# Kernel optimization log

Hardware: AMD Instinct MI355X
Metric: run time of the kernel (lower is better)

Reference implementation:

```python
import jax, jax.numpy as jnp
import numpy as np

S_LEN = 1024; HIDDEN = 2048; VOCAB = 32000; DFF = 6144
NK = 8; NV = 16; DK = 128; DV = 128; CONV_K = 4
CONV_DIM = 2 * NK * DK + NV * DV  # 4096
NQ = 16; NKV = 2; HD = 128; MAX_KV = 4096; SP = 512; CHUNK = 64


def silu(x):
    return x * jax.nn.sigmoid(x)


def rmsnorm(x, w, eps=1e-6):
    xf = x.astype(jnp.float32)
    return (xf * jax.lax.rsqrt(jnp.mean(xf * xf, -1, keepdims=True) + eps)) * w


def gated_rmsnorm(x, z, w, eps=1e-6):
    xf = x.astype(jnp.float32) * silu(z.astype(jnp.float32))
    return (xf * jax.lax.rsqrt(jnp.mean(xf * xf, -1, keepdims=True) + eps)) * w


def rotate_half(x):
    a, b = jnp.split(x, 2, -1)
    return jnp.concatenate([-b, a], -1)


def chunk_gated_delta_rule(q, k, v, g, beta, init_state, chunk=CHUNK):
    # q,k: [B,S,H,Dk]; v: [B,S,H,Dv]; g,beta: [B,S,H]; init_state: [B,H,Dk,Dv]
    q = q / jnp.sqrt(jnp.sum(q * q, -1, keepdims=True) + 1e-6)  # qk l2norm
    k = k / jnp.sqrt(jnp.sum(k * k, -1, keepdims=True) + 1e-6)
    tr = lambda x: x.transpose(0, 2, 1, 3).astype(jnp.float32)
    q, k, v = tr(q), tr(k), tr(v)
    g = g.transpose(0, 2, 1).astype(jnp.float32)
    beta = beta.transpose(0, 2, 1).astype(jnp.float32)
    B, H, S, Dk = q.shape
    Dv = v.shape[-1]
    N = S // chunk  # S is a multiple of chunk here (no padding needed)
    q = q * Dk ** -0.5
    rc = lambda x: x.reshape(B, H, N, chunk, x.shape[-1])
    q, k, v = rc(q), rc(k), rc(v)
    g = jnp.cumsum(g.reshape(B, H, N, chunk), -1)  # cumulative log-decay within chunk
    beta = beta.reshape(B, H, N, chunk)
    kb = k * beta[..., None]
    vb = v * beta[..., None]
    ii = jnp.arange(chunk)
    lower = ii[:, None] >= ii[None, :]
    strict = ii[:, None] > ii[None, :]
    decay = jnp.where(lower, jnp.exp(g[..., :, None] - g[..., None, :]), 0.0)
    # strictly-lower A; T = (I - A)^{-1} (exact triangular solve == converged Neumann series)
    A = -jnp.where(strict, jnp.einsum('bhnik,bhnjk->bhnij', kb, k) * decay, 0.0)
    eye = jnp.eye(chunk, dtype=jnp.float32)
    T = jax.scipy.linalg.solve_triangular(eye - A, jnp.broadcast_to(eye, A.shape), lower=True)
    w = jnp.einsum('bhnij,bhnjd->bhnid', T, vb)
    kc = jnp.einsum('bhnij,bhnjd->bhnid', T, kb * jnp.exp(g)[..., None])
    mv = lambda x: jnp.moveaxis(x, 2, 0)

    def step(state, xs):
        qi, ki, wi, kci, gi, di = xs
        attn = jnp.where(lower, jnp.einsum('bhik,bhjk->bhij', qi, ki) * di, 0.0)
        v_new = wi - jnp.einsum('bhik,bhkd->bhid', kci, state)
        out = jnp.einsum('bhik,bhkd->bhid', qi * jnp.exp(gi)[..., None], state) \
            + jnp.einsum('bhij,bhjd->bhid', attn, v_new)
        gl = gi[..., -1]
        kd = ki * jnp.exp(gl[..., None] - gi)[..., None]
        state = state * jnp.exp(gl)[..., None, None] + jnp.einsum('bhik,bhid->bhkd', kd, v_new)
        return state, out

    final, outs = jax.lax.scan(step, init_state.astype(jnp.float32),
                               (mv(q), mv(k), mv(w), mv(kc), mv(g), mv(decay)))
    out = jnp.moveaxis(outs, 0, 2).reshape(B, H, S, Dv).transpose(0, 2, 1, 3)  # [B,S,H,Dv]
    return out, final


def mlp(x, gw, uw, dw):
    return (silu(x @ gw) * (x @ uw)) @ dw


def model_forward(input_ids, start_pos, rope_cos, rope_sin, attn_mask, conv_state, rec_state,
                  key_cache, value_cache, embed_w, dl_ln_w, dl_qkv_w, conv_w, conv_b, dl_z_w,
                  dl_b_w, dl_a_w, A_log, dt_bias, dn_norm_w, dl_out_w, dl_post_ln_w, dl_gate_w,
                  dl_up_w, dl_down_w, al_ln_w, q_w, q_norm_w, k_w, k_norm_w, v_w, o_w,
                  al_post_ln_w, al_gate_w, al_up_w, al_down_w, final_norm_w, lm_head_w):
    B, S = input_ids.shape
    hidden = embed_w[input_ids]
    # ---------------- DeltaNet (linear attention) layer ----------------
    res = hidden
    x = rmsnorm(hidden, dl_ln_w)
    mixed = (x @ dl_qkv_w).transpose(0, 2, 1)             # [B, CONV_DIM, S]
    padded = jnp.concatenate([conv_state, mixed], -1)      # [B, CONV_DIM, K+S]
    L = padded.shape[-1] - (CONV_K - 1)
    conv = conv_b[:, None] + sum(conv_w[:, kk][:, None] * padded[:, :, kk:kk + L]
                                 for kk in range(CONV_K))  # depthwise conv1d
    mixed = silu(conv[:, :, -S:]).transpose(0, 2, 1)
    new_conv = padded[:, :, -CONV_K:]
    kd = NK * DK
    qq = mixed[..., :kd].reshape(B, S, NK, DK)
    kk_ = mixed[..., kd:2 * kd].reshape(B, S, NK, DK)
    vv = mixed[..., 2 * kd:].reshape(B, S, NV, DV)
    z = (x @ dl_z_w).reshape(B, S, NV, DV)
    beta = jax.nn.sigmoid(x @ dl_b_w)
    a = (x @ dl_a_w).astype(jnp.float32)
    g = -jnp.exp(A_log.astype(jnp.float32)) * jax.nn.softplus(a + dt_bias)
    rep = NV // NK
    qq = jnp.repeat(qq, rep, axis=2)
    kk_ = jnp.repeat(kk_, rep, axis=2)
    core, new_rec = chunk_gated_delta_rule(qq, kk_, vv, g, beta, rec_state)
    core = gated_rmsnorm(core.reshape(-1, DV), z.reshape(-1, DV), dn_norm_w).reshape(B, S, NV * DV)
    hidden = res + core @ dl_out_w
    hidden = hidden + mlp(rmsnorm(hidden, dl_post_ln_w), dl_gate_w, dl_up_w, dl_down_w)
    # ---------------- Full attention layer (gated GQA, KV-cache scatter) ----------------
    res = hidden
    x = rmsnorm(hidden, al_ln_w)
    qg = (x @ q_w).reshape(B, S, NQ, 2 * HD)
    query, gate = jnp.split(qg, 2, -1)
    gate = gate.reshape(B, S, NQ * HD)
    query = rmsnorm(query, q_norm_w).transpose(0, 2, 1, 3)               # [B,NQ,S,HD]
    key_new = rmsnorm((x @ k_w).reshape(B, S, NKV, HD), k_norm_w).transpose(0, 2, 1, 3)
    value_new = (x @ v_w).reshape(B, S, NKV, HD).transpose(0, 2, 1, 3)
    c = rope_cos[:, None]
    sn = rope_sin[:, None]
    query = query * c + rotate_half(query) * sn
    key_new = key_new * c + rotate_half(key_new) * sn
    new_kc = jax.lax.dynamic_update_slice(key_cache, key_new, (0, 0, start_pos, 0))
    new_vc = jax.lax.dynamic_update_slice(value_cache, value_new, (0, 0, start_pos, 0))
    ng = NQ // NKV
    k_rep = jnp.repeat(new_kc, ng, axis=1)
    v_rep = jnp.repeat(new_vc, ng, axis=1)
    scores = jnp.einsum('bhsd,bhtd->bhst', query, k_rep) * HD ** -0.5 + attn_mask
    probs = jax.nn.softmax(scores.astype(jnp.float32), -1).astype(query.dtype)
    ao = jnp.einsum('bhst,bhtd->bhsd', probs, v_rep).transpose(0, 2, 1, 3).reshape(B, S, NQ * HD)
    ao = ao * jax.nn.sigmoid(gate)
    hidden = res + ao @ o_w
    hidden = hidden + mlp(rmsnorm(hidden, al_post_ln_w), al_gate_w, al_up_w, al_down_w)
    logits = rmsnorm(hidden, final_norm_w) @ lm_head_w
    return logits, new_conv, new_rec, new_kc, new_vc


def setup_inputs():
    key = jax.random.key(0)
    ks = iter(jax.random.split(key, 64))
    def rn(shape, s=0.02):
        return jax.random.normal(next(ks), shape, jnp.float32) * s
    input_ids = jax.random.randint(next(ks), (1, S_LEN), 0, VOCAB)
    inv = 1.0 / (10000.0 ** (jnp.arange(0, HD, 2, dtype=jnp.float32) / HD))
    pos = jnp.arange(SP, SP + S_LEN, dtype=jnp.float32)
    fr = pos[:, None] * inv[None, :]
    emb = jnp.concatenate([fr, fr], -1)
    rope_cos = jnp.cos(emb)[None]
    rope_sin = jnp.sin(emb)[None]
    qpos = SP + jnp.arange(S_LEN)
    kpos = jnp.arange(MAX_KV)
    attn_mask = jnp.where(kpos[None, :] <= qpos[:, None], 0.0, -1e9).astype(jnp.float32)[None, None]
    return dict(
        input_ids=input_ids, seq_len=S_LEN, start_pos=SP,
        rope_cos=rope_cos, rope_sin=rope_sin, attn_mask=attn_mask,
        conv_state=rn((1, CONV_DIM, CONV_K), 1.0), rec_state=rn((1, NV, DK, DV), 1.0),
        key_cache=rn((1, NKV, MAX_KV, HD), 1.0), value_cache=rn((1, NKV, MAX_KV, HD), 1.0),
        embed_w=rn((VOCAB, HIDDEN)), dl_ln_w=jnp.ones(HIDDEN),
        dl_qkv_w=rn((HIDDEN, CONV_DIM)), conv_w=rn((CONV_DIM, CONV_K), 0.3),
        conv_b=rn((CONV_DIM,)), dl_z_w=rn((HIDDEN, NV * DV)),
        dl_b_w=rn((HIDDEN, NV)), dl_a_w=rn((HIDDEN, NV)),
        A_log=jnp.log(jnp.linspace(1.0, 8.0, NV)), dt_bias=rn((NV,), 0.1),
        dn_norm_w=jnp.ones(DV), dl_out_w=rn((NV * DV, HIDDEN)),
        dl_post_ln_w=jnp.ones(HIDDEN), dl_gate_w=rn((HIDDEN, DFF)),
        dl_up_w=rn((HIDDEN, DFF)), dl_down_w=rn((DFF, HIDDEN)),
        al_ln_w=jnp.ones(HIDDEN), q_w=rn((HIDDEN, NQ * HD * 2)), q_norm_w=jnp.ones(HD),
        k_w=rn((HIDDEN, NKV * HD)), k_norm_w=jnp.ones(HD), v_w=rn((HIDDEN, NKV * HD)),
        o_w=rn((NQ * HD, HIDDEN)), al_post_ln_w=jnp.ones(HIDDEN),
        al_gate_w=rn((HIDDEN, DFF)), al_up_w=rn((HIDDEN, DFF)), al_down_w=rn((DFF, HIDDEN)),
        final_norm_w=jnp.ones(HIDDEN), lm_head_w=rn((HIDDEN, VOCAB)))


def reference(input_ids, seq_len, start_pos, rope_cos, rope_sin, attn_mask, conv_state,
              rec_state, key_cache, value_cache, embed_w, dl_ln_w, dl_qkv_w, conv_w, conv_b,
              dl_z_w, dl_b_w, dl_a_w, A_log, dt_bias, dn_norm_w, dl_out_w, dl_post_ln_w,
              dl_gate_w, dl_up_w, dl_down_w, al_ln_w, q_w, q_norm_w, k_w, k_norm_w, v_w, o_w,
              al_post_ln_w, al_gate_w, al_up_w, al_down_w, final_norm_w, lm_head_w):
    del seq_len  # unused in original forward body (padding bookkeeping only)
    return model_forward(input_ids, start_pos, rope_cos, rope_sin, attn_mask, conv_state,
                         rec_state, key_cache, value_cache, embed_w, dl_ln_w, dl_qkv_w, conv_w,
                         conv_b, dl_z_w, dl_b_w, dl_a_w, A_log, dt_bias, dn_norm_w, dl_out_w,
                         dl_post_ln_w, dl_gate_w, dl_up_w, dl_down_w, al_ln_w, q_w, q_norm_w,
                         k_w, k_norm_w, v_w, o_w, al_post_ln_w, al_gate_w, al_up_w, al_down_w,
                         final_norm_w, lm_head_w)
```

## Files before the change

### kernel.cpp

```cpp
#include <hip/hip_runtime.h>
#include <math.h>

#define S_LEN 1024
#define HIDN  2048
#define NVH   16
#define CDIM  4096
#define MAXKV 4096
#define SP    512

typedef __attribute__((ext_vector_type(4))) float f32x4v;
typedef _Float16 f16x8 __attribute__((ext_vector_type(8)));
typedef unsigned short ushort_t;

__device__ __forceinline__ unsigned int pack2h(float a, float b) {
  auto h = __builtin_amdgcn_cvt_pkrtz(a, b);
  return __builtin_bit_cast(unsigned int, h);
}
__device__ __forceinline__ ushort_t h16(float x) {
  auto v = __builtin_amdgcn_cvt_pkrtz(x, x);
  return (ushort_t)__builtin_bit_cast(unsigned int, v);
}

template<bool ACC>
__global__ __launch_bounds__(256) void gemm_f16(const float* __restrict__ A,
    const float* __restrict__ B, float* __restrict__ C, int M, int N, int K) {
  __shared__ unsigned int Al[4][128][4];
  __shared__ unsigned int Bl[4][128][4];
  const int tid = threadIdx.x;
  const int gm = M >> 7;
  const int nwg = gridDim.x;
  const int q = nwg >> 3, r = nwg & 7;
  const int xcd = blockIdx.x & 7, ii = blockIdx.x >> 3;
  const int lin = (xcd < r) ? (xcd * (q + 1) + ii)
                            : (r * (q + 1) + (xcd - r) * q + ii);
  const int m0 = (lin % gm) * 128;
  const int n0 = (lin / gm) * 128;
  const int wave = tid >> 6, lane = tid & 63;
  const int wm = (wave >> 1) * 64, wn = (wave & 1) * 64;
  const int lr = lane & 15, lg = lane >> 4;
  const int am = tid >> 1, akb = (tid & 1) * 2;
  const int bn = tid & 127, bkb = (tid >> 7) * 2;
  const float* Ap = A + (size_t)(m0 + am) * K + akb * 8;
  const float* Bp = B + (size_t)(bkb * 8) * N + n0 + bn;
  float ar[16];
  float br[16];
  f32x4v acc[4][4];
  #pragma unroll
  for (int i = 0; i < 4; ++i)
    #pragma unroll
    for (int j = 0; j < 4; ++j)
      #pragma unroll
      for (int r2 = 0; r2 < 4; ++r2) acc[i][j][r2] = 0.f;
  const int NT = K >> 5;
  #pragma unroll
  for (int q2 = 0; q2 < 4; ++q2) *(float4*)&ar[q2 * 4] = *(const float4*)(Ap + q2 * 4);
  #pragma unroll
  for (int j = 0; j < 16; ++j) br[j] = Bp[(size_t)j * N];
  for (int t = 0; t < NT; ++t) {
    __syncthreads();
    *(uint4*)&Al[akb][am][0] = make_uint4(
        pack2h(ar[0], ar[1]), pack2h(ar[2], ar[3]),
        pack2h(ar[4], ar[5]), pack2h(ar[6], ar[7]));
    *(uint4*)&Al[akb + 1][am][0] = make_uint4(
        pack2h(ar[8], ar[9]), pack2h(ar[10], ar[11]),
        pack2h(ar[12], ar[13]), pack2h(ar[14], ar[15]));
    *(uint4*)&Bl[bkb][bn][0] = make_uint4(
        pack2h(br[0], br[1]), pack2h(br[2], br[3]),
        pack2h(br[4], br[5]), pack2h(br[6], br[7]));
    *(uint4*)&Bl[bkb + 1][bn][0] = make_uint4(
        pack2h(br[8], br[9]), pack2h(br[10], br[11]),
        pack2h(br[12], br[13]), pack2h(br[14], br[15]));
    if (t + 1 < NT) {
      Ap += 32; Bp += (size_t)32 * N;
      #pragma unroll
      for (int q2 = 0; q2 < 4; ++q2) *(float4*)&ar[q2 * 4] = *(const float4*)(Ap + q2 * 4);
      #pragma unroll
      for (int j = 0; j < 16; ++j) br[j] = Bp[(size_t)j * N];
    }
    __syncthreads();
    f16x8 af[4], bfr[4];
    #pragma unroll
    for (int mi = 0; mi < 4; ++mi)
      af[mi] = *(const f16x8*)&Al[lg][wm + mi * 16 + lr][0];
    #pragma unroll
    for (int ni = 0; ni < 4; ++ni)
      bfr[ni] = *(const f16x8*)&Bl[lg][wn + ni * 16 + lr][0];
    #pragma unroll
    for (int mi = 0; mi < 4; ++mi)
      #pragma unroll
      for (int ni = 0; ni < 4; ++ni)
        acc[mi][ni] = __builtin_amdgcn_mfma_f32_16x16x32_f16(
            af[mi], bfr[ni], acc[mi][ni], 0, 0, 0);
  }
  #pragma unroll
  for (int mi = 0; mi < 4; ++mi) {
    #pragma unroll
    for (int ni = 0; ni < 4; ++ni) {
      const int rr = m0 + wm + mi * 16 + lg * 4;
      const int cc = n0 + wn + ni * 16 + lr;
      #pragma unroll
      for (int r2 = 0; r2 < 4; ++r2) {
        float* cp = C + (size_t)(rr + r2) * N + cc;
        if (ACC) *cp += acc[mi][ni][r2];
        else     *cp = acc[mi][ni][r2];
      }
    }
  }
}

__global__ __launch_bounds__(256) void embed_k(const int* __restrict__ ids,
    const float* __restrict__ emb, float* __restrict__ hid) {
  int t = blockIdx.x * 256 + threadIdx.x;
  int s = t >> 9;
  int c4 = (t & 511) * 4;
  *(float4*)(hid + (size_t)s * HIDN + c4) =
      *(const float4*)(emb + (size_t)ids[s] * HIDN + c4);
}

__global__ __launch_bounds__(256) void rmsnorm_k(const float* __restrict__ in,
    const float* __restrict__ w, float* __restrict__ out) {
  const int row = blockIdx.x;
  const float* ip = in + (size_t)row * HIDN;
  float ss = 0.f;
  for (int c = threadIdx.x * 4; c < HIDN; c += 1024) {
    float4 v = *(const float4*)(ip + c);
    ss += v.x * v.x + v.y * v.y + v.z * v.z + v.w * v.w;
  }
  #pragma unroll
  for (int o = 32; o > 0; o >>= 1) ss += __shfl_down(ss, o, 64);
  __shared__ float sred[4];
  if ((threadIdx.x & 63) == 0) sred[threadIdx.x >> 6] = ss;
  __syncthreads();
  float tot = sred[0] + sred[1] + sred[2] + sred[3];
  float sc = 1.f / sqrtf(tot * (1.f / HIDN) + 1e-6f);
  for (int c = threadIdx.x * 4; c < HIDN; c += 1024) {
    float4 v = *(const float4*)(ip + c);
    float4 o = make_float4(v.x * sc * w[c], v.y * sc * w[c + 1],
                           v.z * sc * w[c + 2], v.w * sc * w[c + 3]);
    *(float4*)(out + (size_t)row * HIDN + c) = o;
  }
}

__global__ __launch_bounds__(256) void newconv_k(const float* __restrict__ mixed,
                                                 float* __restrict__ nc) {
  int t = blockIdx.x * 256 + threadIdx.x;
  int c = t >> 2, kk = t & 3;
  nc[t] = mixed[(size_t)(1020 + kk) * CDIM + c];
}

__global__ __launch_bounds__(256) void conv_k(const float* __restrict__ mixed,
    const float* __restrict__ cstate, const float* __restrict__ cw,
    const float* __restrict__ cb, float* __restrict__ convo) {
  int idx = blockIdx.x * 256 + threadIdx.x;
  int c = idx & (CDIM - 1);
  int s = idx >> 12;
  float acc = cb[c];
  #pragma unroll
  for (int kk = 0; kk < 4; ++kk) {
    int j = s + 1 + kk;
    float pv = (j < 4) ? cstate[c * 4 + j] : mixed[(size_t)(j - 4) * CDIM + c];
    acc = fmaf(cw[c * 4 + kk], pv, acc);
  }
  convo[(size_t)s * CDIM + c] = acc / (1.f + expf(-acc));
}

__global__ __launch_bounds__(128) void qknorm_k(const float* __restrict__ convo,
    float* __restrict__ qn, float* __restrict__ kn) {
  const int b = blockIdx.x;
  const int h8 = b & 7, s = b >> 3;
  const int d = threadIdx.x;
  float qv = convo[(size_t)s * CDIM + h8 * 128 + d];
  float kv = convo[(size_t)s * CDIM + 1024 + h8 * 128 + d];
  __shared__ float sred[4];
  float pq = qv * qv, pk = kv * kv;
  #pragma unroll
  for (int o = 32; o > 0; o >>= 1) { pq += __shfl_down(pq, o, 64); pk += __shfl_down(pk, o, 64); }
  if ((d & 63) == 0) { sred[d >> 6] = pq; sred[2 + (d >> 6)] = pk; }
  __syncthreads();
  float sq = sred[0] + sred[1], sk = sred[2] + sred[3];
  qn[((size_t)h8 * S_LEN + s) * 128 + d] = qv * (1.f / sqrtf(sq + 1e-6f)) * 0.08838834764831845f;
  kn[((size_t)h8 * S_LEN + s) * 128 + d] = kv * (1.f / sqrtf(sk + 1e-6f));
}

__global__ __launch_bounds__(256) void betag_k(const float* __restrict__ x,
    const float* __restrict__ bw, const float* __restrict__ aw,
    const float* __restrict__ A_log, const float* __restrict__ dt_bias,
    float* __restrict__ beta, float* __restrict__ g) {
  __shared__ float sx[2048];
  __shared__ float rb[16][17], ra[16][17];
  const int s = blockIdx.x;
  for (int c = threadIdx.x; c < HIDN; c += 256) sx[c] = x[(size_t)s * HIDN + c];
  __syncthreads();
  const int h = threadIdx.x & 15, part = threadIdx.x >> 4;
  float accb = 0.f, acca = 0.f;
  for (int j = 0; j < 128; ++j) {
    int k = part * 128 + j;
    float xv = sx[k];
    accb = fmaf(xv, bw[(size_t)k * 16 + h], accb);
    acca = fmaf(xv, aw[(size_t)k * 16 + h], acca);
  }
  rb[part][h] = accb; ra[part][h] = acca;
  __syncthreads();
  if (threadIdx.x < 16) {
    const int hh = threadIdx.x;
    float sb = 0.f, sa = 0.f;
    for (int p = 0; p < 16; ++p) { sb += rb[p][hh]; sa += ra[p][hh]; }
    beta[(size_t)s * 16 + hh] = 1.f / (1.f + expf(-sb));
    float aa = sa + dt_bias[hh];
    float sp = (aa > 20.f) ? aa : log1pf(expf(aa));
    g[(size_t)s * 16 + hh] = -expf(A_log[hh]) * sp;
  }
}

__global__ __launch_bounds__(256) void delta_phase1(
    const float* __restrict__ qn, const float* __restrict__ kn,
    const float* __restrict__ convo, const float* __restrict__ beta,
    const float* __restrict__ g,
    float* __restrict__ Wb, ushort_t* __restrict__ KC16,
    ushort_t* __restrict__ Q16, ushort_t* __restrict__ K16,
    ushort_t* __restrict__ ATT16, float* __restrict__ GCb) {
  __shared__ float sK[64][129];
  __shared__ float sV[64][129];
  __shared__ float sQ[64][129];
  __shared__ float sT[64][64];
  __shared__ float sgc[64], sbeta[64], seg[64], sEgl[64];
  const int blk = blockIdx.x;
  const int n = blk & 15, h = blk >> 4;
  const int hq = h >> 1;
  const int r0 = n * 64;
  const int tid = threadIdx.x;
  const size_t hn = (size_t)h * 16 + n;
  for (int t = tid; t < 2048; t += 256) {
    int i = t >> 5, c4 = (t & 31) * 4;
    float4 kv = *(const float4*)(kn + ((size_t)hq * S_LEN + r0 + i) * 128 + c4);
    float4 qv = *(const float4*)(qn + ((size_t)hq * S_LEN + r0 + i) * 128 + c4);
    float4 vv = *(const float4*)(convo + (size_t)(r0 + i) * CDIM + 2048 + h * 128 + c4);
    sK[i][c4+0]=kv.x; sK[i][c4+1]=kv.y; sK[i][c4+2]=kv.z; sK[i][c4+3]=kv.w;
    sQ[i][c4+0]=qv.x; sQ[i][c4+1]=qv.y; sQ[i][c4+2]=qv.z; sQ[i][c4+3]=qv.w;
    sV[i][c4+0]=vv.x; sV[i][c4+1]=vv.y; sV[i][c4+2]=vv.z; sV[i][c4+3]=vv.w;
  }
  if (tid < 64) sbeta[tid] = beta[(size_t)(r0 + tid) * NVH + h];
  __syncthreads();
  if (tid == 0) {
    float acc = 0.f;
    for (int i = 0; i < 64; ++i) { acc += g[(size_t)(r0 + i) * NVH + h]; sgc[i] = acc; }
  }
  __syncthreads();
  if (tid < 64) {
    seg[tid] = expf(sgc[tid]);
    sEgl[tid] = expf(sgc[63] - sgc[tid]);
  }
  {
    const int ty = tid >> 4, tx = tid & 15;
    float a[4][4] = {};
    #pragma unroll 4
    for (int k = 0; k < 128; ++k) {
      float kr[4], kc_[4];
      #pragma unroll
      for (int di = 0; di < 4; ++di) kr[di] = sK[ty * 4 + di][k];
      #pragma unroll
      for (int dj = 0; dj < 4; ++dj) kc_[dj] = sK[tx * 4 + dj][k];
      #pragma unroll
      for (int di = 0; di < 4; ++di)
        #pragma unroll
        for (int dj = 0; dj < 4; ++dj)
          a[di][dj] = fmaf(kr[di], kc_[dj], a[di][dj]);
    }
    #pragma unroll
    for (int di = 0; di < 4; ++di) {
      int i = ty * 4 + di;
      #pragma unroll
      for (int dj = 0; dj < 4; ++dj) {
        int j = tx * 4 + dj;
        float v;
        if (i > j) v = sbeta[i] * a[di][dj] * expf(sgc[i] - sgc[j]);
        else v = (i == j) ? 1.f : 0.f;
        sT[i][j] = v;
      }
    }
  }
  __syncthreads();
  for (int i = 1; i < 64; ++i) {
    float acc = 0.f;
    const int c = tid;
    const bool act = (c < 64 && c <= i);
    if (act) {
      acc = (c == i) ? 1.f : 0.f;
      for (int j = c; j < i; ++j) acc -= sT[i][j] * sT[j][c];
    }
    __syncthreads();
    if (act) sT[i][c] = acc;
    __syncthreads();
  }
  for (int t = tid; t < 1024; t += 256) {
    int i = t >> 4, dg = (t & 15) * 8;
    float aw[8] = {}, ak[8] = {};
    for (int j = 0; j <= i; ++j) {
      float tv = sT[i][j] * sbeta[j];
      float te = tv * seg[j];
      #pragma unroll
      for (int u = 0; u < 8; ++u) {
        aw[u] = fmaf(tv, sV[j][dg + u], aw[u]);
        ak[u] = fmaf(te, sK[j][dg + u], ak[u]);
      }
    }
    float* wp = Wb + (hn * 64 + i) * 128 + dg;
    *(float4*)wp = make_float4(aw[0], aw[1], aw[2], aw[3]);
    *(float4*)(wp + 4) = make_float4(aw[4], aw[5], aw[6], aw[7]);
    uint4 kc = make_uint4(pack2h(-ak[0], -ak[1]), pack2h(-ak[2], -ak[3]),
                          pack2h(-ak[4], -ak[5]), pack2h(-ak[6], -ak[7]));
    *(uint4*)(KC16 + hn * 8192 + (dg >> 3) * 512 + i * 8) = kc;
  }
  for (int t = tid; t < 1024; t += 256) {
    int i = t >> 4, dg = (t & 15) * 8;
    float e = seg[i];
    uint4 qv = make_uint4(
        pack2h(sQ[i][dg] * e, sQ[i][dg + 1] * e),
        pack2h(sQ[i][dg + 2] * e, sQ[i][dg + 3] * e),
        pack2h(sQ[i][dg + 4] * e, sQ[i][dg + 5] * e),
        pack2h(sQ[i][dg + 6] * e, sQ[i][dg + 7] * e));
    *(uint4*)(Q16 + hn * 8192 + (dg >> 3) * 512 + i * 8) = qv;
  }
  for (int t = tid; t < 1024; t += 256) {
    int kv = t & 127, ib = t >> 7;
    int i0 = ib * 8;
    uint4 kk2 = make_uint4(
        pack2h(sK[i0 + 0][kv] * sEgl[i0 + 0], sK[i0 + 1][kv] * sEgl[i0 + 1]),
        pack2h(sK[i0 + 2][kv] * sEgl[i0 + 2], sK[i0 + 3][kv] * sEgl[i0 + 3]),
        pack2h(sK[i0 + 4][kv] * sEgl[i0 + 4], sK[i0 + 5][kv] * sEgl[i0 + 5]),
        pack2h(sK[i0 + 6][kv] * sEgl[i0 + 6], sK[i0 + 7][kv] * sEgl[i0 + 7]));
    *(uint4*)(K16 + hn * 8192 + ib * 1024 + kv * 8) = kk2;
  }
  __syncthreads();
  {
    const int ty = tid >> 4, tx = tid & 15;
    float a[4][4] = {};
    #pragma unroll 4
    for (int k = 0; k < 128; ++k) {
      float qr[4], kc_[4];
      #pragma unroll
      for (int di = 0; di < 4; ++di) qr[di] = sQ[ty * 4 + di][k];
      #pragma unroll
      for (int dj = 0; dj < 4; ++dj) kc_[dj] = sK[tx * 4 + dj][k];
      #pragma unroll
      for (int di = 0; di < 4; ++di)
        #pragma unroll
        for (int dj = 0; dj < 4; ++dj)
          a[di][dj] = fmaf(qr[di], kc_[dj], a[di][dj]);
    }
    #pragma unroll
    for (int di = 0; di < 4; ++di) {
      int i = ty * 4 + di;
      #pragma unroll
      for (int dj = 0; dj < 4; ++dj) {
        int j = tx * 4 + dj;
        float v = 0.f;
        if (i >= j) v = a[di][dj] * expf(sgc[i] - sgc[j]);
        sT[i][j] = v;
      }
    }
  }
  __syncthreads();
  for (int t = tid; t < 512; t += 256) {
    int i = t >> 3, jb = t & 7;
    const float* ap = &sT[i][jb * 8];
    uint4 av = make_uint4(pack2h(ap[0], ap[1]), pack2h(ap[2], ap[3]),
                          pack2h(ap[4], ap[5]), pack2h(ap[6], ap[7]));
    *(uint4*)(ATT16 + hn * 4096 + jb * 512 + i * 8) = av;
  }
  if (tid < 64) GCb[hn * 64 + tid] = sgc[tid];
}

__global__ __launch_bounds__(256) void delta_phase2(
    const ushort_t* __restrict__ KC16, const ushort_t* __restrict__ Q16,
    const ushort_t* __restrict__ K16, const ushort_t* __restrict__ ATT16,
    const float* __restrict__ Wb, const float* __restrict__ GCb,
    const float* __restrict__ rec_state,
    float* __restrict__ core, float* __restrict__ new_rec) {
  __shared__ uint4 bufKC[1024];
  __shared__ uint4 bufQ[1024];
  __shared__ uint4 bufK[1024];
  __shared__ uint4 bufA[512];
  __shared__ uint4 bufS[512];
  __shared__ uint4 bufV[256];
  ushort_t* sKC = (ushort_t*)bufKC;
  ushort_t* sQ6 = (ushort_t*)bufQ;
  ushort_t* sK6 = (ushort_t*)bufK;
  ushort_t* sAT = (ushort_t*)bufA;
  ushort_t* sS  = (ushort_t*)bufS;
  ushort_t* sVn = (ushort_t*)bufV;
  const int h = blockIdx.x >> 2, ds = blockIdx.x & 3;
  const int d0 = ds * 32;
  const int tid = threadIdx.x;
  const int w = tid >> 6;
  const int lane = tid & 63, lr = lane & 15, lg = lane >> 4;
  const int rowS0 = w * 32;
  f32x4v aS[2][2];
  #pragma unroll
  for (int tm = 0; tm < 2; ++tm)
    #pragma unroll
    for (int tn = 0; tn < 2; ++tn)
      #pragma unroll
      for (int r = 0; r < 4; ++r) {
        int row = rowS0 + tm * 16 + lg * 4 + r;
        int col = tn * 16 + lr;
        aS[tm][tn][r] = rec_state[((size_t)h * 128 + row) * 128 + d0 + col];
      }
  for (int n = 0; n < 16; ++n) {
    const size_t hn = (size_t)h * 16 + n;
    const uint4* pKC = (const uint4*)(KC16 + hn * 8192);
    const uint4* pQ  = (const uint4*)(Q16  + hn * 8192);
    const uint4* pK  = (const uint4*)(K16  + hn * 8192);
    const uint4* pA  = (const uint4*)(ATT16 + hn * 4096);
    uint4 stKC[4], stQ[4], stK[4], stA[2];
    #pragma unroll
    for (int u = 0; u < 4; ++u) {
      stKC[u] = pKC[tid + u * 256];
      stQ[u]  = pQ[tid + u * 256];
      stK[u]  = pK[tid + u * 256];
    }
    #pragma unroll
    for (int u = 0; u < 2; ++u) stA[u] = pA[tid + u * 256];
    const float egl = expf(GCb[hn * 64 + 63]);
    float wseed[2][4];
    #pragma unroll
    for (int tn = 0; tn < 2; ++tn)
      #pragma unroll
      for (int r = 0; r < 4; ++r)
        wseed[tn][r] = Wb[(hn * 64 + (w * 16 + lg * 4 + r)) * 128 + d0 + tn * 16 + lr];
    #pragma unroll
    for (int tm = 0; tm < 2; ++tm)
      #pragma unroll
      for (int tn = 0; tn < 2; ++tn)
        #pragma unroll
        for (int r = 0; r < 4; ++r) {
          int row = rowS0 + tm * 16 + lg * 4 + r;
          int col = tn * 16 + lr;
          sS[(row >> 3) * 256 + col * 8 + (row & 7)] = h16(aS[tm][tn][r]);
        }
    #pragma unroll
    for (int u = 0; u < 4; ++u) {
      bufKC[tid + u * 256] = stKC[u];
      bufQ[tid + u * 256]  = stQ[u];
      bufK[tid + u * 256]  = stK[u];
    }
    #pragma unroll
    for (int u = 0; u < 2; ++u) bufA[tid + u * 256] = stA[u];
    __syncthreads();
    f32x4v aV[2];
    #pragma unroll
    for (int tn = 0; tn < 2; ++tn)
      #pragma unroll
      for (int r = 0; r < 4; ++r) aV[tn][r] = wseed[tn][r];
    #pragma unroll
    for (int c = 0; c < 4; ++c) {
      f16x8 a = *(const f16x8*)&sKC[((c * 4 + lg) * 64 + w * 16 + lr) * 8];
      #pragma unroll
      for (int tn = 0; tn < 2; ++tn) {
        f16x8 b = *(const f16x8*)&sS[((c * 4 + lg) * 32 + tn * 16 + lr) * 8];
        aV[tn] = __builtin_amdgcn_mfma_f32_16x16x32_f16(a, b, aV[tn], 0, 0, 0);
      }
    }
    #pragma unroll
    for (int tn = 0; tn < 2; ++tn)
      #pragma unroll
      for (int r = 0; r < 4; ++r) {
        int row = w * 16 + lg * 4 + r;
        int col = tn * 16 + lr;
        sVn[(row >> 3) * 256 + col * 8 + (row & 7)] = h16(aV[tn][r]);
      }
    __syncthreads();
    f32x4v aO[2];
    #pragma unroll
    for (int tn = 0; tn < 2; ++tn)
      #pragma unroll
      for (int r = 0; r < 4; ++r) aO[tn][r] = 0.f;
    #pragma unroll
    for (int c = 0; c < 4; ++c) {
      f16x8 a = *(const f16x8*)&sQ6[((c * 4 + lg) * 64 + w * 16 + lr) * 8];
      #pragma unroll
      for (int tn = 0; tn < 2; ++tn) {
        f16x8 b = *(const f16x8*)&sS[((c * 4 + lg) * 32 + tn * 16 + lr) * 8];
        aO[tn] = __builtin_amdgcn_mfma_f32_16x16x32_f16(a, b, aO[tn], 0, 0, 0);
      }
    }
    #pragma unroll
    for (int c = 0; c < 2; ++c) {
      f16x8 a = *(const f16x8*)&sAT[((c * 4 + lg) * 64 + w * 16 + lr) * 8];
      #pragma unroll
      for (int tn = 0; tn < 2; ++tn) {
        f16x8 b = *(const f16x8*)&sVn[((c * 4 + lg) * 32 + tn * 16 + lr) * 8];
        aO[tn] = __builtin_amdgcn_mfma_f32_16x16x32_f16(a, b, aO[tn], 0, 0, 0);
      }
    }
    #pragma unroll
    for (int tn = 0; tn < 2; ++tn)
      #pragma unroll
      for (int r = 0; r < 4; ++r) {
        int row = w * 16 + lg * 4 + r;
        core[(size_t)(n * 64 + row) * HIDN + h * 128 + d0 + tn * 16 + lr] = aO[tn][r];
      }
    #pragma unroll
    for (int tm = 0; tm < 2; ++tm)
      #pragma unroll
      for (int tn = 0; tn < 2; ++tn)
        #pragma unroll
        for (int r = 0; r < 4; ++r) aS[tm][tn][r] *= egl;
    #pragma unroll
    for (int tm = 0; tm < 2; ++tm) {
      #pragma unroll
      for (int c = 0; c < 2; ++c) {
        f16x8 a = *(const f16x8*)&sK6[((c * 4 + lg) * 128 + rowS0 + tm * 16 + lr) * 8];
        #pragma unroll
        for (int tn = 0; tn < 2; ++tn) {
          f16x8 b = *(const f16x8*)&sVn[((c * 4 + lg) * 32 + tn * 16 + lr) * 8];
          aS[tm][tn] = __builtin_amdgcn_mfma_f32_16x16x32_f16(a, b, aS[tm][tn], 0, 0, 0);
        }
      }
    }
    __syncthreads();
  }
  #pragma unroll
  for (int tm = 0; tm < 2; ++tm)
    #pragma unroll
    for (int tn = 0; tn < 2; ++tn)
      #pragma unroll
      for (int r = 0; r < 4; ++r) {
        int row = rowS0 + tm * 16 + lg * 4 + r;
        int col = tn * 16 + lr;
        new_rec[((size_t)h * 128 + row) * 128 + d0 + col] = aS[tm][tn][r];
      }
}

__global__ __launch_bounds__(128) void gatedrms_k(float* __restrict__ core,
    const float* __restrict__ z, const float* __restrict__ w) {
  const int b = blockIdx.x;
  const int h = b & 15, s = b >> 4;
  const int d = threadIdx.x;
  size_t idx = (size_t)s * HIDN + h * 128 + d;
  float cv = core[idx], zv = z[idx];
  float xf = cv * (zv / (1.f + expf(-zv)));
  __shared__ float sred[2];
  float ps = xf * xf;
  #pragma unroll
  for (int o = 32; o > 0; o >>= 1) ps += __shfl_down(ps, o, 64);
  if ((d & 63) == 0) sred[d >> 6] = ps;
  __syncthreads();
  float ss = sred[0] + sred[1];
  core[idx] = xf * (1.f / sqrtf(ss * (1.f / 128.f) + 1e-6f)) * w[d];
}

__global__ __launch_bounds__(256) void silumul_k(float* __restrict__ gbuf,
                                                 const float* __restrict__ ubuf) {
  int t = blockIdx.x * 256 + threadIdx.x;
  float4 gv = ((const float4*)gbuf)[t];
  float4 uv = ((const float4*)ubuf)[t];
  gv.x = gv.x / (1.f + expf(-gv.x)) * uv.x;
  gv.y = gv.y / (1.f + expf(-gv.y)) * uv.y;
  gv.z = gv.z / (1.f + expf(-gv.z)) * uv.z;
  gv.w = gv.w / (1.f + expf(-gv.w)) * uv.w;
  ((float4*)gbuf)[t] = gv;
}

__global__ __launch_bounds__(128) void qrope_k(const float* __restrict__ qg,
    const float* __restrict__ qnw, const float* __restrict__ cosb,
    const float* __restrict__ sinb, float* __restrict__ qhat,
    float* __restrict__ agate) {
  const int b = blockIdx.x;
  const int h = b & 15, s = b >> 4;
  const int d = threadIdx.x;
  float qv = qg[(size_t)s * 4096 + h * 256 + d];
  float gv = qg[(size_t)s * 4096 + h * 256 + 128 + d];
  __shared__ float sred[2];
  float ps = qv * qv;
  #pragma unroll
  for (int o = 32; o > 0; o >>= 1) ps += __shfl_down(ps, o, 64);
  if ((d & 63) == 0) sred[d >> 6] = ps;
  __syncthreads();
  float ss = sred[0] + sred[1];
  float qn_ = qv * (1.f / sqrtf(ss * (1.f / 128.f) + 1e-6f)) * qnw[d];
  __shared__ float tmp[128];
  tmp[d] = qn_;
  __syncthreads();
  float other = tmp[d ^ 64];
  float rh = (d < 64) ? -other : other;
  float c = cosb[(size_t)s * 128 + d];
  float sn = sinb[(size_t)s * 128 + d];
  qhat[((size_t)h * S_LEN + s) * 128 + d] = qn_ * c + rh * sn;
  agate[(size_t)s * HIDN + h * 128 + d] = gv;
}

__global__ __launch_bounds__(128) void kvrope_k(const float* __restrict__ kraw,
    const float* __restrict__ vraw, const float* __restrict__ knw,
    const float* __restrict__ cosb, const float* __restrict__ sinb,
    float* __restrict__ kcache, float* __restrict__ vcache) {
  const int b = blockIdx.x;
  const int h2 = b & 1, s = b >> 1;
  const int d = threadIdx.x;
  float kv = kraw[(size_t)s * 256 + h2 * 128 + d];
  __shared__ float sred[2];
  float ps = kv * kv;
  #pragma unroll
  for (int o = 32; o > 0; o >>= 1) ps += __shfl_down(ps, o, 64);
  if ((d & 63) == 0) sred[d >> 6] = ps;
  __syncthreads();
  float ss = sred[0] + sred[1];
  float kn_ = kv * (1.f / sqrtf(ss * (1.f / 128.f) + 1e-6f)) * knw[d];
  __shared__ float tmp[128];
  tmp[d] = kn_;
  __syncthreads();
  float other = tmp[d ^ 64];
  float rh = (d < 64) ? -other : other;
  size_t row = (size_t)h2 * MAXKV + SP + s;
  kcache[row * 128 + d] = kn_ * cosb[(size_t)s * 128 + d] + rh * sinb[(size_t)s * 128 + d];
  vcache[row * 128 + d] = vraw[(size_t)s * 256 + h2 * 128 + d];
}

__global__ __launch_bounds__(256) void attn_k(const float* __restrict__ qhat,
    const float* __restrict__ kcache, const float* __restrict__ vcache,
    const float* __restrict__ agate, float* __restrict__ ao) {
  __shared__ unsigned int Ql[16][64][4];
  __shared__ unsigned int Kl[16][64][4];
  __shared__ unsigned int Vl[8][128][4];
  __shared__ unsigned int Pl[8][64][4];
  const int h = blockIdx.x >> 4, qb = blockIdx.x & 15;
  const int hkv = h >> 3;
  const int tid = threadIdx.x;
  const int wave = tid >> 6, lane = tid & 63;
  const int lr = lane & 15, lg = lane >> 4;
  const float SCALE = 0.08838834764831845f;
  const float* Qb = qhat + ((size_t)h * S_LEN + qb * 64) * 128;
  #pragma unroll
  for (int it = 0; it < 4; ++it) {
    int tt = tid + it * 256;
    int row = tt >> 4, kb = tt & 15;
    float4 a = *(const float4*)(Qb + row * 128 + kb * 8);
    float4 b = *(const float4*)(Qb + row * 128 + kb * 8 + 4);
    *(uint4*)&Ql[kb][row][0] = make_uint4(
        pack2h(a.x * SCALE, a.y * SCALE), pack2h(a.z * SCALE, a.w * SCALE),
        pack2h(b.x * SCALE, b.y * SCALE), pack2h(b.z * SCALE, b.w * SCALE));
  }
  float m_run[4], l_run[4];
  #pragma unroll
  for (int r = 0; r < 4; ++r) { m_run[r] = -3.0e38f; l_run[r] = 0.f; }
  f32x4v accO[8];
  #pragma unroll
  for (int nd = 0; nd < 8; ++nd)
    #pragma unroll
    for (int r = 0; r < 4; ++r) accO[nd][r] = 0.f;
  const int ntiles = 9 + qb;
  for (int kt = 0; kt < ntiles; ++kt) {
    __syncthreads();
    const float* Kb = kcache + ((size_t)hkv * MAXKV + kt * 64) * 128;
    const float* Vb = vcache + ((size_t)hkv * MAXKV + kt * 64) * 128;
    #pragma unroll
    for (int it = 0; it < 4; ++it) {
      int tt = tid + it * 256;
      int row = tt >> 4, kb = tt & 15;
      float4 a = *(const float4*)(Kb + row * 128 + kb * 8);
      float4 b = *(const float4*)(Kb + row * 128 + kb * 8 + 4);
      *(uint4*)&Kl[kb][row][0] = make_uint4(
          pack2h(a.x, a.y), pack2h(a.z, a.w), pack2h(b.x, b.y), pack2h(b.z, b.w));
    }
    #pragma unroll
    for (int it = 0; it < 4; ++it) {
      int tt = tid + it * 256;
      int key = tt >> 4, dg = tt & 15;
      float4 a = *(const float4*)(Vb + key * 128 + dg * 8);
      float4 b = *(const float4*)(Vb + key * 128 + dg * 8 + 4);
      _Float16* vp = (_Float16*)Vl;
      int base = (key >> 3) * 1024 + (key & 7);
      vp[base + (dg * 8 + 0) * 8] = (_Float16)a.x;
      vp[base + (dg * 8 + 1) * 8] = (_Float16)a.y;
      vp[base + (dg * 8 + 2) * 8] = (_Float16)a.z;
      vp[base + (dg * 8 + 3) * 8] = (_Float16)a.w;
      vp[base + (dg * 8 + 4) * 8] = (_Float16)b.x;
      vp[base + (dg * 8 + 5) * 8] = (_Float16)b.y;
      vp[base + (dg * 8 + 6) * 8] = (_Float16)b.z;
      vp[base + (dg * 8 + 7) * 8] = (_Float16)b.w;
    }
    __syncthreads();
    f32x4v accS[4];
    #pragma unroll
    for (int ni = 0; ni < 4; ++ni)
      #pragma unroll
      for (int r = 0; r < 4; ++r) accS[ni][r] = 0.f;
    #pragma unroll
    for (int c = 0; c < 4; ++c) {
      f16x8 aq = *(const f16x8*)&Ql[c * 4 + lg][wave * 16 + lr][0];
      #pragma unroll
      for (int ni = 0; ni < 4; ++ni) {
        f16x8 bk = *(const f16x8*)&Kl[c * 4 + lg][ni * 16 + lr][0];
        accS[ni] = __builtin_amdgcn_mfma_f32_16x16x32_f16(aq, bk, accS[ni], 0, 0, 0);
      }
    }
    const bool boundary = (kt == ntiles - 1);
    float alpha[4];
    #pragma unroll
    for (int r = 0; r < 4; ++r) {
      const int qrow = wave * 16 + lg * 4 + r;
      float tm = -3.0e38f;
      #pragma unroll
      for (int ni = 0; ni < 4; ++ni) {
        if (boundary && (ni * 16 + lr) > qrow) accS[ni][r] = -3.0e38f;
        tm = fmaxf(tm, accS[ni][r]);
      }
      tm = fmaxf(tm, __shfl_xor(tm, 1, 64));
      tm = fmaxf(tm, __shfl_xor(tm, 2, 64));
      tm = fmaxf(tm, __shfl_xor(tm, 4, 64));
      tm = fmaxf(tm, __shfl_xor(tm, 8, 64));
      float mnew = fmaxf(m_run[r], tm);
      alpha[r] = expf(m_run[r] - mnew);
      m_run[r] = mnew;
      float ls = 0.f;
      #pragma unroll
      for (int ni = 0; ni < 4; ++ni) {
        float p = expf(accS[ni][r] - mnew);
        accS[ni][r] = p;
        ls += p;
      }
      ls += __shfl_xor(ls, 1, 64);
      ls += __shfl_xor(ls, 2, 64);
      ls += __shfl_xor(ls, 4, 64);
      ls += __shfl_xor(ls, 8, 64);
      l_run[r] = l_run[r] * alpha[r] + ls;
    }
    {
      _Float16* pp = (_Float16*)Pl;
      #pragma unroll
      for (int ni = 0; ni < 4; ++ni) {
        int key = ni * 16 + lr;
        int base = (key >> 3) * 512 + (key & 7);
        #pragma unroll
        for (int r = 0; r < 4; ++r) {
          int q = wave * 16 + lg * 4 + r;
          pp[base + q * 8] = (_Float16)accS[ni][r];
        }
      }
    }
    #pragma unroll
    for (int nd = 0; nd < 8; ++nd)
      #pragma unroll
      for (int r = 0; r < 4; ++r) accO[nd][r] *= alpha[r];
    #pragma unroll
    for (int c2 = 0; c2 < 2; ++c2) {
      f16x8 ap = *(const f16x8*)&Pl[c2 * 4 + lg][wave * 16 + lr][0];
      #pragma unroll
      for (int nd = 0; nd < 8; ++nd) {
        f16x8 bv = *(const f16x8*)&Vl[c2 * 4 + lg][nd * 16 + lr][0];
        accO[nd] = __builtin_amdgcn_mfma_f32_16x16x32_f16(ap, bv, accO[nd], 0, 0, 0);
      }
    }
  }
  #pragma unroll
  for (int r = 0; r < 4; ++r) {
    const int s = qb * 64 + wave * 16 + lg * 4 + r;
    const float inv = 1.f / l_run[r];
    #pragma unroll
    for (int nd = 0; nd < 8; ++nd) {
      int d = nd * 16 + lr;
      float gv = agate[(size_t)s * HIDN + h * 128 + d];
      ao[(size_t)s * HIDN + h * 128 + d] = accO[nd][r] * inv * (1.f / (1.f + expf(-gv)));
    }
  }
}

static inline void gemm(const float* A, const float* B, float* C,
                        int M, int N, int K, bool acc, hipStream_t st) {
  dim3 g((N / 128) * (M / 128));
  if (acc) hipLaunchKernelGGL((gemm_f16<true>),  g, dim3(256), 0, st, A, B, C, M, N, K);
  else     hipLaunchKernelGGL((gemm_f16<false>), g, dim3(256), 0, st, A, B, C, M, N, K);
}

extern "C" void kernel_launch(void* const* d_in, const int* in_sizes, int n_in,
                              void* d_out, int out_size, void* d_ws, size_t ws_size,
                              hipStream_t stream) {
  (void)in_sizes; (void)n_in; (void)out_size; (void)ws_size;
  const int*   ids         = (const int*)  d_in[0];
  const float* rope_cos    = (const float*)d_in[3];
  const float* rope_sin    = (const float*)d_in[4];
  const float* conv_state  = (const float*)d_in[6];
  const float* rec_state   = (const float*)d_in[7];
  const float* key_cache   = (const float*)d_in[8];
  const float* value_cache = (const float*)d_in[9];
  const float* embed_w     = (const float*)d_in[10];
  const float* dl_ln_w     = (const float*)d_in[11];
  const float* dl_qkv_w    = (const float*)d_in[12];
  const float* conv_w      = (const float*)d_in[13];
  const float* conv_b      = (const float*)d_in[14];
  const float* dl_z_w      = (const float*)d_in[15];
  const float* dl_b_w      = (const float*)d_in[16];
  const float* dl_a_w      = (const float*)d_in[17];
  const float* A_log       = (const float*)d_in[18];
  const float* dt_bias     = (const float*)d_in[19];
  const float* dn_norm_w   = (const float*)d_in[20];
  const float* dl_out_w    = (const float*)d_in[21];
  const float* dl_post_ln  = (const float*)d_in[22];
  const float* dl_gate_w   = (const float*)d_in[23];
  const float* dl_up_w     = (const float*)d_in[24];
  const float* dl_down_w   = (const float*)d_in[25];
  const float* al_ln_w     = (const float*)d_in[26];
  const float* q_w         = (const float*)d_in[27];
  const float* q_norm_w    = (const float*)d_in[28];
  const float* k_w         = (const float*)d_in[29];
  const float* k_norm_w    = (const float*)d_in[30];
  const float* v_w         = (const float*)d_in[31];
  const float* o_w         = (const float*)d_in[32];
  const float* al_post_ln  = (const float*)d_in[33];
  const float* al_gate_w   = (const float*)d_in[34];
  const float* al_up_w     = (const float*)d_in[35];
  const float* al_down_w   = (const float*)d_in[36];
  const float* final_norm  = (const float*)d_in[37];
  const float* lm_head_w   = (const float*)d_in[38];

  float* out = (float*)d_out;
  float* logits   = out;
  float* new_conv = out + 32768000;
  float* new_rec  = out + 32784384;
  float* new_kc   = out + 33046528;
  float* new_vc   = out + 34095104;

  float* A_mixed = logits;
  float* A_convo = logits + 4194304;
  float* A_z     = logits + 8388608;
  float* A_qn    = logits + 10485760;
  float* A_kn    = logits + 11534336;
  float* A_w     = logits + 12582912;
  float* A_kc    = logits + 14680064;
  float* A_att   = logits + 16777216;
  float* A_gc    = logits + 17825792;
  float* A_core  = logits + 17842176;
  float* A_big0  = logits + 19939328;
  float* A_big1  = logits + 26230784;
  float* A_qhat  = A_big1;
  float* A_gate  = A_big1 + 2097152;
  float* A_ao    = A_big1 + 4194304;
  float* A_kraw  = A_mixed;
  float* A_vraw  = A_mixed + 262144;

  ushort_t* KC16  = (ushort_t*)A_kc;
  ushort_t* K16   = (ushort_t*)A_kc + 2097152;
  ushort_t* Q16   = (ushort_t*)A_att;
  ushort_t* ATT16 = (ushort_t*)A_big0;

  float* ws     = (float*)d_ws;
  float* W_hid  = ws;
  float* W_x    = ws + 2097152;
  float* W_beta = ws + 4194304;
  float* W_g    = ws + 4210688;

  hipLaunchKernelGGL(embed_k, dim3(2048), dim3(256), 0, stream, ids, embed_w, W_hid);
  hipLaunchKernelGGL(rmsnorm_k, dim3(1024), dim3(256), 0, stream, W_hid, dl_ln_w, W_x);
  gemm(W_x, dl_qkv_w, A_mixed, 1024, 4096, 2048, false, stream);
  hipLaunchKernelGGL(newconv_k, dim3(64), dim3(256), 0, stream, A_mixed, new_conv);
  hipLaunchKernelGGL(conv_k, dim3(16384), dim3(256), 0, stream,
                     A_mixed, conv_state, conv_w, conv_b, A_convo);
  gemm(W_x, dl_z_w, A_z, 1024, 2048, 2048, false, stream);
  hipLaunchKernelGGL(betag_k, dim3(1024), dim3(256), 0, stream,
                     W_x, dl_b_w, dl_a_w, A_log, dt_bias, W_beta, W_g);
  hipLaunchKernelGGL(qknorm_k, dim3(8192), dim3(128), 0, stream, A_convo, A_qn, A_kn);
  hipLaunchKernelGGL(delta_phase1, dim3(256), dim3(256), 0, stream,
                     A_qn, A_kn, A_convo, W_beta, W_g,
                     A_w, KC16, Q16, K16, ATT16, A_gc);
  hipLaunchKernelGGL(delta_phase2, dim3(64), dim3(256), 0, stream,
                     KC16, Q16, K16, ATT16, A_w, A_gc, rec_state, A_core, new_rec);
  hipLaunchKernelGGL(gatedrms_k, dim3(16384), dim3(128), 0, stream, A_core, A_z, dn_norm_w);
  gemm(A_core, dl_out_w, W_hid, 1024, 2048, 2048, true, stream);
  hipLaunchKernelGGL(rmsnorm_k, dim3(1024), dim3(256), 0, stream, W_hid, dl_post_ln, W_x);
  gemm(W_x, dl_gate_w, A_big0, 1024, 6144, 2048, false, stream);
  gemm(W_x, dl_up_w,   A_big1, 1024, 6144, 2048, false, stream);
  hipLaunchKernelGGL(silumul_k, dim3(6144), dim3(256), 0, stream, A_big0, A_big1);
  gemm(A_big0, dl_down_w, W_hid, 1024, 2048, 6144, true, stream);
  hipLaunchKernelGGL(rmsnorm_k, dim3(1024), dim3(256), 0, stream, W_hid, al_ln_w, W_x);
  gemm(W_x, q_w, A_big0, 1024, 4096, 2048, false, stream);
  hipLaunchKernelGGL(qrope_k, dim3(16384), dim3(128), 0, stream,
                     A_big0, q_norm_w, rope_cos, rope_sin, A_qhat, A_gate);
  gemm(W_x, k_w, A_kraw, 1024, 256, 2048, false, stream);
  gemm(W_x, v_w, A_vraw, 1024, 256, 2048, false, stream);
  hipMemcpyAsync(new_kc, key_cache,   (size_t)2 * MAXKV * 128 * 4, hipMemcpyDeviceToDevice, stream);
  hipMemcpyAsync(new_vc, value_cache, (size_t)2 * MAXKV * 128 * 4, hipMemcpyDeviceToDevice, stream);
  hipLaunchKernelGGL(kvrope_k, dim3(2048), dim3(128), 0, stream,
                     A_kraw, A_vraw, k_norm_w, rope_cos, rope_sin, new_kc, new_vc);
  hipLaunchKernelGGL(attn_k, dim3(256), dim3(256), 0, stream,
                     A_qhat, new_kc, new_vc, A_gate, A_ao);
  gemm(A_ao, o_w, W_hid, 1024, 2048, 2048, true, stream);
  hipLaunchKernelGGL(rmsnorm_k, dim3(1024), dim3(256), 0, stream, W_hid, al_post_ln, W_x);
  gemm(W_x, al_gate_w, A_big0, 1024, 6144, 2048, false, stream);
  gemm(W_x, al_up_w,   A_big1, 1024, 6144, 2048, false, stream);
  hipLaunchKernelGGL(silumul_k, dim3(6144), dim3(256), 0, stream, A_big0, A_big1);
  gemm(A_big0, al_down_w, W_hid, 1024, 2048, 6144, true, stream);
  hipLaunchKernelGGL(rmsnorm_k, dim3(1024), dim3(256), 0, stream, W_hid, final_norm, W_x);
  gemm(W_x, lm_head_w, logits, 1024, 32000, 2048, false, stream);
}
```

Before: 1.719 ms.

## Pre-convert weights to tiled fp16 and stream B tiles directly into LDS

Before each GEMM, a new kernel converts that layer's fp32 weight matrix into a pre-tiled fp16 buffer held in a large device global. The GEMM then loads B tiles with global_load_lds 16-byte direct-to-LDS copies instead of strided per-column fp32 loads plus in-register packing. This targets the uncoalesced, repeated fp32 weight reads that every row-tile block performed. The cost is an extra full read of all fp32 weights and an fp16 write every call, about 343 MB of added device global state, and reliance on correct vmcnt waits before the barrier for the async LDS loads.

Result: slower. 2.032 ms (+18.2%).

```diff
diff --git a/kernel.cpp b/kernel.cpp
--- a/kernel.cpp
+++ b/kernel.cpp
@@ -12,6 +12,9 @@
 typedef _Float16 f16x8 __attribute__((ext_vector_type(8)));
 typedef unsigned short ushort_t;
 
+#define W16_TOTAL 171442176ULL
+__device__ ushort_t g_W16[W16_TOTAL];
+
 __device__ __forceinline__ unsigned int pack2h(float a, float b) {
   auto h = __builtin_amdgcn_cvt_pkrtz(a, b);
   return __builtin_bit_cast(unsigned int, h);
@@ -20,12 +23,40 @@
   auto v = __builtin_amdgcn_cvt_pkrtz(x, x);
   return (ushort_t)__builtin_bit_cast(unsigned int, v);
 }
+__device__ __forceinline__ void gload16(const void* g, void* l) {
+  __builtin_amdgcn_global_load_lds(
+      (const __attribute__((address_space(1))) void*)(g),
+      (__attribute__((address_space(3))) void*)(l), 16, 0, 0);
+}
+
+__global__ __launch_bounds__(256) void convw_k(const float* __restrict__ W,
+    size_t off, int K, int N, int total) {
+  int t = blockIdx.x * 256 + threadIdx.x;
+  if (t >= total) return;
+  int n_glob = t % N;
+  int kb_glob = t / N;
+  int kt = kb_glob >> 2, kb = kb_glob & 3;
+  int np = n_glob >> 7, n = n_glob & 127;
+  const float* src = W + (size_t)(kt * 32 + kb * 8) * N + n_glob;
+  float v0 = src[0];
+  float v1 = src[(size_t)N];
+  float v2 = src[(size_t)2 * N];
+  float v3 = src[(size_t)3 * N];
+  float v4 = src[(size_t)4 * N];
+  float v5 = src[(size_t)5 * N];
+  float v6 = src[(size_t)6 * N];
+  float v7 = src[(size_t)7 * N];
+  uint4 o = make_uint4(pack2h(v0, v1), pack2h(v2, v3),
+                       pack2h(v4, v5), pack2h(v6, v7));
+  *(uint4*)(g_W16 + off + ((size_t)np * (K >> 5) + kt) * 4096
+            + (size_t)((kb << 7) + n) * 8) = o;
+}
 
 template<bool ACC>
 __global__ __launch_bounds__(256) void gemm_f16(const float* __restrict__ A,
-    const float* __restrict__ B, float* __restrict__ C, int M, int N, int K) {
+    size_t bOff, float* __restrict__ C, int M, int N, int K) {
   __shared__ unsigned int Al[4][128][4];
-  __shared__ unsigned int Bl[4][128][4];
+  __shared__ unsigned int Bl[2048];
   const int tid = threadIdx.x;
   const int gm = M >> 7;
   const int nwg = gridDim.x;
@@ -39,11 +70,9 @@
   const int wm = (wave >> 1) * 64, wn = (wave & 1) * 64;
   const int lr = lane & 15, lg = lane >> 4;
   const int am = tid >> 1, akb = (tid & 1) * 2;
-  const int bn = tid & 127, bkb = (tid >> 7) * 2;
   const float* Ap = A + (size_t)(m0 + am) * K + akb * 8;
-  const float* Bp = B + (size_t)(bkb * 8) * N + n0 + bn;
+  const ushort_t* Bt = g_W16 + bOff + (size_t)(n0 >> 7) * (K >> 5) * 4096;
   float ar[16];
-  float br[16];
   f32x4v acc[4][4];
   #pragma unroll
   for (int i = 0; i < 4; ++i)
@@ -54,28 +83,26 @@
   const int NT = K >> 5;
   #pragma unroll
   for (int q2 = 0; q2 < 4; ++q2) *(float4*)&ar[q2 * 4] = *(const float4*)(Ap + q2 * 4);
-  #pragma unroll
-  for (int j = 0; j < 16; ++j) br[j] = Bp[(size_t)j * N];
   for (int t = 0; t < NT; ++t) {
     __syncthreads();
+    {
+      const ushort_t* bs = Bt + (size_t)t * 4096;
+      #pragma unroll
+      for (int i2 = 0; i2 < 2; ++i2) {
+        int c = wave * 2 + i2;
+        gload16(bs + c * 512 + lane * 8, &Bl[c * 256]);
+      }
+    }
     *(uint4*)&Al[akb][am][0] = make_uint4(
         pack2h(ar[0], ar[1]), pack2h(ar[2], ar[3]),
         pack2h(ar[4], ar[5]), pack2h(ar[6], ar[7]));
     *(uint4*)&Al[akb + 1][am][0] = make_uint4(
         pack2h(ar[8], ar[9]), pack2h(ar[10], ar[11]),
         pack2h(ar[12], ar[13]), pack2h(ar[14], ar[15]));
-    *(uint4*)&Bl[bkb][bn][0] = make_uint4(
-        pack2h(br[0], br[1]), pack2h(br[2], br[3]),
-        pack2h(br[4], br[5]), pack2h(br[6], br[7]));
-    *(uint4*)&Bl[bkb + 1][bn][0] = make_uint4(
-        pack2h(br[8], br[9]), pack2h(br[10], br[11]),
-        pack2h(br[12], br[13]), pack2h(br[14], br[15]));
     if (t + 1 < NT) {
-      Ap += 32; Bp += (size_t)32 * N;
+      Ap += 32;
       #pragma unroll
       for (int q2 = 0; q2 < 4; ++q2) *(float4*)&ar[q2 * 4] = *(const float4*)(Ap + q2 * 4);
-      #pragma unroll
-      for (int j = 0; j < 16; ++j) br[j] = Bp[(size_t)j * N];
     }
     __syncthreads();
     f16x8 af[4], bfr[4];
@@ -84,7 +111,7 @@
       af[mi] = *(const f16x8*)&Al[lg][wm + mi * 16 + lr][0];
     #pragma unroll
     for (int ni = 0; ni < 4; ++ni)
-      bfr[ni] = *(const f16x8*)&Bl[lg][wn + ni * 16 + lr][0];
+      bfr[ni] = *(const f16x8*)&Bl[(lg * 128 + wn + ni * 16 + lr) * 4];
     #pragma unroll
     for (int mi = 0; mi < 4; ++mi)
       #pragma unroll
@@ -765,11 +792,31 @@
   }
 }
 
-static inline void gemm(const float* A, const float* B, float* C,
+#define OFF_QKV 0ULL
+#define OFF_Z   8388608ULL
+#define OFF_OUT 12582912ULL
+#define OFF_G1  16777216ULL
+#define OFF_U1  29360128ULL
+#define OFF_D1  41943040ULL
+#define OFF_Q   54525952ULL
+#define OFF_K   62914560ULL
+#define OFF_V   63438848ULL
+#define OFF_O   63963136ULL
+#define OFF_G2  68157440ULL
+#define OFF_U2  80740352ULL
+#define OFF_D2  93323264ULL
+#define OFF_LM  105906176ULL
+
+static inline void convw(const float* W, size_t off, int K, int N, hipStream_t st) {
+  int total = (K >> 3) * N;
+  hipLaunchKernelGGL(convw_k, dim3((total + 255) / 256), dim3(256), 0, st,
+                     W, off, K, N, total);
+}
+static inline void gemm(const float* A, size_t bOff, float* C,
                         int M, int N, int K, bool acc, hipStream_t st) {
   dim3 g((N / 128) * (M / 128));
-  if (acc) hipLaunchKernelGGL((gemm_f16<true>),  g, dim3(256), 0, st, A, B, C, M, N, K);
-  else     hipLaunchKernelGGL((gemm_f16<false>), g, dim3(256), 0, st, A, B, C, M, N, K);
+  if (acc) hipLaunchKernelGGL((gemm_f16<true>),  g, dim3(256), 0, st, A, bOff, C, M, N, K);
+  else     hipLaunchKernelGGL((gemm_f16<false>), g, dim3(256), 0, st, A, bOff, C, M, N, K);
 }
 
 extern "C" void kernel_launch(void* const* d_in, const int* in_sizes, int n_in,
@@ -851,11 +898,13 @@
 
   hipLaunchKernelGGL(embed_k, dim3(2048), dim3(256), 0, stream, ids, embed_w, W_hid);
   hipLaunchKernelGGL(rmsnorm_k, dim3(1024), dim3(256), 0, stream, W_hid, dl_ln_w, W_x);
-  gemm(W_x, dl_qkv_w, A_mixed, 1024, 4096, 2048, false, stream);
+  convw(dl_qkv_w, OFF_QKV, 2048, 4096, stream);
+  gemm(W_x, OFF_QKV, A_mixed, 1024, 4096, 2048, false, stream);
   hipLaunchKernelGGL(newconv_k, dim3(64), dim3(256), 0, stream, A_mixed, new_conv);
   hipLaunchKernelGGL(conv_k, dim3(16384), dim3(256), 0, stream,
                      A_mixed, conv_state, conv_w, conv_b, A_convo);
-  gemm(W_x, dl_z_w, A_z, 1024, 2048, 2048, false, stream);
+  convw(dl_z_w, OFF_Z, 2048, 2048, stream);
+  gemm(W_x, OFF_Z, A_z, 1024, 2048, 2048, false, stream);
   hipLaunchKernelGGL(betag_k, dim3(1024), dim3(256), 0, stream,
                      W_x, dl_b_w, dl_a_w, A_log, dt_bias, W_beta, W_g);
   hipLaunchKernelGGL(qknorm_k, dim3(8192), dim3(128), 0, stream, A_convo, A_qn, A_kn);
@@ -865,30 +914,42 @@
   hipLaunchKernelGGL(delta_phase2, dim3(64), dim3(256), 0, stream,
                      KC16, Q16, K16, ATT16, A_w, A_gc, rec_state, A_core, new_rec);
   hipLaunchKernelGGL(gatedrms_k, dim3(16384), dim3(128), 0, stream, A_core, A_z, dn_norm_w);
-  gemm(A_core, dl_out_w, W_hid, 1024, 2048, 2048, true, stream);
+  convw(dl_out_w, OFF_OUT, 2048, 2048, stream);
+  gemm(A_core, OFF_OUT, W_hid, 1024, 2048, 2048, true, stream);
   hipLaunchKernelGGL(rmsnorm_k, dim3(1024), dim3(256), 0, stream, W_hid, dl_post_ln, W_x);
-  gemm(W_x, dl_gate_w, A_big0, 1024, 6144, 2048, false, stream);
-  gemm(W_x, dl_up_w,   A_big1, 1024, 6144, 2048, false, stream);
+  convw(dl_gate_w, OFF_G1, 2048, 6144, stream);
+  gemm(W_x, OFF_G1, A_big0, 1024, 6144, 2048, false, stream);
+  convw(dl_up_w, OFF_U1, 2048, 6144, stream);
+  gemm(W_x, OFF_U1, A_big1, 1024, 6144, 2048, false, stream);
   hipLaunchKernelGGL(silumul_k, dim3(6144), dim3(256), 0, stream, A_big0, A_big1);
-  gemm(A_big0, dl_down_w, W_hid, 1024, 2048, 6144, true, stream);
+  convw(dl_down_w, OFF_D1, 6144, 2048, stream);
+  gemm(A_big0, OFF_D1, W_hid, 1024, 2048, 6144, true, stream);
   hipLaunchKernelGGL(rmsnorm_k, dim3(1024), dim3(256), 0, stream, W_hid, al_ln_w, W_x);
-  gemm(W_x, q_w, A_big0, 1024, 4096, 2048, false, stream);
+  convw(q_w, OFF_Q, 2048, 4096, stream);
+  gemm(W_x, OFF_Q, A_big0, 1024, 4096, 2048, false, stream);
   hipLaunchKernelGGL(qrope_k, dim3(16384), dim3(128), 0, stream,
                      A_big0, q_norm_w, rope_cos, rope_sin, A_qhat, A_gate);
-  gemm(W_x, k_w, A_kraw, 1024, 256, 2048, false, stream);
-  gemm(W_x, v_w, A_vraw, 1024, 256, 2048, false, stream);
+  convw(k_w, OFF_K, 2048, 256, stream);
+  gemm(W_x, OFF_K, A_kraw, 1024, 256, 2048, false, stream);
+  convw(v_w, OFF_V, 2048, 256, stream);
+  gemm(W_x, OFF_V, A_vraw, 1024, 256, 2048, false, stream);
   hipMemcpyAsync(new_kc, key_cache,   (size_t)2 * MAXKV * 128 * 4, hipMemcpyDeviceToDevice, stream);
   hipMemcpyAsync(new_vc, value_cache, (size_t)2 * MAXKV * 128 * 4, hipMemcpyDeviceToDevice, stream);
   hipLaunchKernelGGL(kvrope_k, dim3(2048), dim3(128), 0, stream,
                      A_kraw, A_vraw, k_norm_w, rope_cos, rope_sin, new_kc, new_vc);
   hipLaunchKernelGGL(attn_k, dim3(256), dim3(256), 0, stream,
                      A_qhat, new_kc, new_vc, A_gate, A_ao);
-  gemm(A_ao, o_w, W_hid, 1024, 2048, 2048, true, stream);
+  convw(o_w, OFF_O, 2048, 2048, stream);
+  gemm(A_ao, OFF_O, W_hid, 1024, 2048, 2048, true, stream);
   hipLaunchKernelGGL(rmsnorm_k, dim3(1024), dim3(256), 0, stream, W_hid, al_post_ln, W_x);
-  gemm(W_x, al_gate_w, A_big0, 1024, 6144, 2048, false, stream);
-  gemm(W_x, al_up_w,   A_big1, 1024, 6144, 2048, false, stream);
+  convw(al_gate_w, OFF_G2, 2048, 6144, stream);
+  gemm(W_x, OFF_G2, A_big0, 1024, 6144, 2048, false, stream);
+  convw(al_up_w, OFF_U2, 2048, 6144, stream);
+  gemm(W_x, OFF_U2, A_big1, 1024, 6144, 2048, false, stream);
   hipLaunchKernelGGL(silumul_k, dim3(6144), dim3(256), 0, stream, A_big0, A_big1);
-  gemm(A_big0, al_down_w, W_hid, 1024, 2048, 6144, true, stream);
+  convw(al_down_w, OFF_D2, 6144, 2048, stream);
+  gemm(A_big0, OFF_D2, W_hid, 1024, 2048, 6144, true, stream);
   hipLaunchKernelGGL(rmsnorm_k, dim3(1024), dim3(256), 0, stream, W_hid, final_norm, W_x);
-  gemm(W_x, lm_head_w, logits, 1024, 32000, 2048, false, stream);
-}
+  convw(lm_head_w, OFF_LM, 2048, 32000, stream);
+  gemm(W_x, OFF_LM, logits, 1024, 32000, 2048, false, stream);
+}
```
